# Kernel tuning notes

Measured on AMD Instinct MI355X. Metric: run time of the kernel, lower is better.

## Reference

```python
import math
import jax, jax.numpy as jnp
import numpy as np

WINDOW = 2  # LocalAttention default window_size
EPS = 1e-6


def _linear(x, W, b):
    return x @ W + b


def local_attention(x, Wq, bq, Wk, bk, Wv, bv):
    # x: [B, S, D]
    B, S, D = x.shape
    q = _linear(x, Wq, bq)
    k = _linear(x, Wk, bk)
    v = _linear(x, Wv, bv)
    idx = jnp.arange(S)
    # 0/1 banded mask -> softmax gives a dense row-stochastic matrix (faithful to source)
    mask = (jnp.abs(idx[:, None] - idx[None, :]) <= WINDOW).astype(x.dtype)  # [S, S]
    A = jax.nn.softmax(mask, axis=-1)  # [S, S]
    kk = jnp.einsum('st,btd->bsd', A, k)  # bmm(A, k)
    scores = jnp.einsum('bsd,btd->bst', q, kk) / math.sqrt(D)
    return jnp.einsum('bst,btd->bsd', jax.nn.softmax(scores, axis=-1), v)


def whole_norm(x, w, b):
    # LayerNorm with normalized_shape == full [B, S, D]: normalize over ALL elements
    mu = jnp.mean(x)
    var = jnp.mean(jnp.square(x - mu))
    return (x - mu) * jax.lax.rsqrt(var + EPS) * w + b


def ffn(x, W1, b1, W2, b2):
    return _linear(jax.nn.relu(_linear(x, W1, b1)), W2, b2)


def branch(feat, Wq, bq, Wk, bk, Wv, bv, W1, b1, W2, b2, nw, nb):
    out = local_attention(feat, Wq, bq, Wk, bk, Wv, bv)
    out = whole_norm(out + feat, nw, nb)
    out = ffn(out, W1, b1, W2, b2)
    return whole_norm(out + feat, nw, nb)


def _make_params(key, B, S, D):
    ks = jax.random.split(key, 5)
    s = 1.0 / math.sqrt(D)
    Wq = jax.random.normal(ks[0], (D, D), jnp.float32) * s
    Wk = jax.random.normal(ks[1], (D, D), jnp.float32) * s
    Wv = jax.random.normal(ks[2], (D, D), jnp.float32) * s
    W1 = jax.random.normal(ks[3], (D, 4 * D), jnp.float32) * s
    W2 = jax.random.normal(ks[4], (4 * D, D), jnp.float32) * (1.0 / math.sqrt(4 * D))
    return dict(Wq=Wq, bq=jnp.zeros((D,)), Wk=Wk, bk=jnp.zeros((D,)),
                Wv=Wv, bv=jnp.zeros((D,)), W1=W1, b1=jnp.zeros((4 * D,)),
                W2=W2, b2=jnp.zeros((D,)), nw=jnp.ones((B, S, D)), nb=jnp.zeros((B, S, D)))


def setup_inputs() -> dict:
    key = jax.random.key(0)
    k0, k1, k2, k3 = jax.random.split(key, 4)
    B, St, Dt = 8, 512, 1024
    Si, Di = 196, 768
    inp = {
        'text_feature': jax.random.normal(k0, (B, St, Dt), jnp.float32),
        'image_feature': jax.random.normal(k1, (B, Si, Di), jnp.float32),
    }
    tp = _make_params(k2, B, St, Dt)
    ip = _make_params(k3, B, Si, Di)
    for k, v in tp.items():
        inp['t_' + k] = v
    for k, v in ip.items():
        inp['i_' + k] = v
    return inp


def reference(text_feature, image_feature,
              t_Wq, t_bq, t_Wk, t_bk, t_Wv, t_bv, t_W1, t_b1, t_W2, t_b2, t_nw, t_nb,
              i_Wq, i_bq, i_Wk, i_bk, i_Wv, i_bv, i_W1, i_b1, i_W2, i_b2, i_nw, i_nb):
    image_out = branch(image_feature, i_Wq, i_bq, i_Wk, i_bk, i_Wv, i_bv,
                       i_W1, i_b1, i_W2, i_b2, i_nw, i_nb)
    text_out = branch(text_feature, t_Wq, t_bq, t_Wk, t_bk, t_Wv, t_bv,
                      t_W1, t_b1, t_W2, t_b2, t_nw, t_nb)
    return (text_out, image_out)
```

## Files before the change

kernel.cpp:

```cpp
#include <hip/hip_runtime.h>
#include <math.h>

typedef float  f32x4  __attribute__((ext_vector_type(4)));
typedef short  bf16x8 __attribute__((ext_vector_type(8)));

__device__ __forceinline__ unsigned short f2bf(float f) {
    union { float f; unsigned u; } v; v.f = f;
    unsigned u = v.u;
    return (unsigned short)((u + 0x7FFFu + ((u >> 16) & 1u)) >> 16);
}
__device__ __forceinline__ float bf2f(unsigned short u) {
    union { unsigned u; float f; } v; v.u = (unsigned)u << 16; return v.f;
}

#define GLOAD_LDS16(g, l)                                                      \
    __builtin_amdgcn_global_load_lds(                                          \
        (const __attribute__((address_space(1))) void*)(g),                    \
        (__attribute__((address_space(3))) void*)(l), 16, 0, 0)

template<int MR, int NR, bool OUT_BF16, bool RELU>
__global__ __launch_bounds__(512, 2)
void gemm2_bf16(const unsigned short* __restrict__ A,
                const unsigned short* __restrict__ BT,
                const float* __restrict__ bias, void* __restrict__ Cv,
                int M, int N, int K, int lda, int ldb, int ldc,
                long long sA, long long sB, long long sC, float alpha,
                int gx, int gy)
{
    constexpr int BK = 32;
    constexpr int WM = MR * 16, WN = NR * 16;
    constexpr int BM = 2 * WM, BN = 4 * WN;
    __shared__ unsigned short Asm[2][BM * BK];
    __shared__ unsigned short Bsm[2][BN * BK];

    A  += (long long)blockIdx.z * sA;
    BT += (long long)blockIdx.z * sB;
    char* Cb = (char*)Cv + (long long)blockIdx.z * sC * (OUT_BF16 ? 2 : 4);

    const int nwg = gx * gy;
    int orig = blockIdx.x;
    int xcd = orig & 7, sidx = orig >> 3;
    int qq = nwg >> 3, rr = nwg & 7;
    int wg = (xcd < rr ? xcd * (qq + 1) : rr * (qq + 1) + (xcd - rr) * qq) + sidx;
    const int row0 = (wg % gy) * BM;
    const int col0 = (wg / gy) * BN;

    const int tid  = threadIdx.x;
    const int lane = tid & 63;
    const int wave = tid >> 6;
    const int wr   = wave >> 2;
    const int wc   = wave & 3;

    const int srow = tid >> 2;
    const int skel = (tid & 3) * 8;

    const int lrow = lane & 15;
    const int lk   = (lane >> 4) * 8;

    f32x4 acc[MR][NR] = {};

    auto stage = [&](int buf, int k0) {
        #pragma unroll
        for (int is = 0; is < BM / 128; ++is)
            GLOAD_LDS16(A + (long long)(row0 + is * 128 + srow) * lda + (k0 + skel),
                        &Asm[buf][(is * 128 + srow) * BK + skel]);
        #pragma unroll
        for (int is = 0; is < BN / 128; ++is)
            GLOAD_LDS16(BT + (long long)(col0 + is * 128 + srow) * ldb + (k0 + skel),
                        &Bsm[buf][(is * 128 + srow) * BK + skel]);
    };

    const int nt = K / BK;
    stage(0, 0);
    __syncthreads();
    int cur = 0;
    for (int t = 0; t < nt; ++t) {
        if (t + 1 < nt) stage(cur ^ 1, (t + 1) * BK);

        bf16x8 af[MR], bfr[NR];
        #pragma unroll
        for (int mf = 0; mf < MR; ++mf)
            af[mf] = *(const bf16x8*)&Asm[cur][(wr * WM + mf * 16 + lrow) * BK + lk];
        #pragma unroll
        for (int nf = 0; nf < NR; ++nf)
            bfr[nf] = *(const bf16x8*)&Bsm[cur][(wc * WN + nf * 16 + lrow) * BK + lk];
        #pragma unroll
        for (int mf = 0; mf < MR; ++mf)
            #pragma unroll
            for (int nf = 0; nf < NR; ++nf)
                acc[mf][nf] = __builtin_amdgcn_mfma_f32_16x16x32_bf16(
                    af[mf], bfr[nf], acc[mf][nf], 0, 0, 0);

        __syncthreads();
        cur ^= 1;
    }

    const int crow = (lane >> 4) * 4;
    const int ccol = lane & 15;
    #pragma unroll
    for (int mf = 0; mf < MR; ++mf) {
        int rbase = row0 + wr * WM + mf * 16 + crow;
        #pragma unroll
        for (int nf = 0; nf < NR; ++nf) {
            int c = col0 + wc * WN + nf * 16 + ccol;
            if (c >= N) continue;
            float bv = bias ? bias[c] : 0.f;
            #pragma unroll
            for (int j = 0; j < 4; ++j) {
                int r = rbase + j;
                if (r >= M) continue;
                float v = acc[mf][nf][j] * alpha + bv;
                if (RELU) v = fmaxf(v, 0.f);
                if (OUT_BF16)
                    ((unsigned short*)Cb)[(long long)r * ldc + c] = f2bf(v);
                else
                    ((float*)Cb)[(long long)r * ldc + c] = v;
            }
        }
    }
}

template<int MR, int NR>
static void gemm2_t(bool outBf16, bool relu,
                    const unsigned short* A, const unsigned short* BT, const float* bias,
                    void* C, int M, int N, int K, int lda, int ldb, int ldc,
                    int batch, long long sA, long long sB, long long sC,
                    float alpha, hipStream_t st)
{
    const int BM = 2 * MR * 16, BN = 4 * NR * 16;
    int gx = (N + BN - 1) / BN, gy = (M + BM - 1) / BM;
    dim3 grid(gx * gy, 1, batch);
    if (outBf16) {
        if (relu) gemm2_bf16<MR, NR, true , true ><<<grid, 512, 0, st>>>(A, BT, bias, C, M, N, K, lda, ldb, ldc, sA, sB, sC, alpha, gx, gy);
        else      gemm2_bf16<MR, NR, true , false><<<grid, 512, 0, st>>>(A, BT, bias, C, M, N, K, lda, ldb, ldc, sA, sB, sC, alpha, gx, gy);
    } else {
        if (relu) gemm2_bf16<MR, NR, false, true ><<<grid, 512, 0, st>>>(A, BT, bias, C, M, N, K, lda, ldb, ldc, sA, sB, sC, alpha, gx, gy);
        else      gemm2_bf16<MR, NR, false, false><<<grid, 512, 0, st>>>(A, BT, bias, C, M, N, K, lda, ldb, ldc, sA, sB, sC, alpha, gx, gy);
    }
}

template<int BM, int BN, bool OUT_BF16>
__global__ __launch_bounds__(256)
void gemm_bf16(const unsigned short* __restrict__ A,
               const unsigned short* __restrict__ BT,
               const float* __restrict__ bias, void* __restrict__ Cv,
               int M, int N, int K, int lda, int ldb, int ldc,
               long long sA, long long sB, long long sC, float alpha,
               int gx, int gy)
{
    constexpr int BK = 32;
    constexpr int WM = BM / 2, WN = BN / 2;
    constexpr int MR = WM / 16, NR = WN / 16;
    __shared__ unsigned short Asm[BM * BK];
    __shared__ unsigned short Bsm[BN * BK];

    A  += (long long)blockIdx.z * sA;
    BT += (long long)blockIdx.z * sB;
    char* Cb = (char*)Cv + (long long)blockIdx.z * sC * (OUT_BF16 ? 2 : 4);

    const int nwg = gx * gy;
    int orig = blockIdx.x;
    int xcd = orig & 7, sidx = orig >> 3;
    int qq = nwg >> 3, rr = nwg & 7;
    int wg = (xcd < rr ? xcd * (qq + 1) : rr * (qq + 1) + (xcd - rr) * qq) + sidx;
    const int row0 = (wg % gy) * BM;
    const int col0 = (wg / gy) * BN;

    const int tid  = threadIdx.x;
    const int lane = tid & 63;
    const int wave = tid >> 6;
    const int wr   = wave >> 1;
    const int wc   = wave & 1;

    const int srow = tid >> 2;
    const int skel = (tid & 3) * 8;

    f32x4 acc[MR][NR] = {};

    const int lrow = lane & 15;
    const int lk   = (lane >> 4) * 8;

    for (int k0 = 0; k0 < K; k0 += BK) {
        #pragma unroll
        for (int is = 0; is < BM / 64; ++is)
            GLOAD_LDS16(A + (long long)(row0 + is * 64 + srow) * lda + (k0 + skel),
                        &Asm[(is * 64 + srow) * BK + skel]);
        #pragma unroll
        for (int is = 0; is < BN / 64; ++is)
            GLOAD_LDS16(BT + (long long)(col0 + is * 64 + srow) * ldb + (k0 + skel),
                        &Bsm[(is * 64 + srow) * BK + skel]);
        __syncthreads();

        bf16x8 af[MR], bfr[NR];
        #pragma unroll
        for (int mf = 0; mf < MR; ++mf)
            af[mf] = *(const bf16x8*)&Asm[(wr * WM + mf * 16 + lrow) * BK + lk];
        #pragma unroll
        for (int nf = 0; nf < NR; ++nf)
            bfr[nf] = *(const bf16x8*)&Bsm[(wc * WN + nf * 16 + lrow) * BK + lk];
        #pragma unroll
        for (int mf = 0; mf < MR; ++mf)
            #pragma unroll
            for (int nf = 0; nf < NR; ++nf)
                acc[mf][nf] = __builtin_amdgcn_mfma_f32_16x16x32_bf16(
                    af[mf], bfr[nf], acc[mf][nf], 0, 0, 0);
        __syncthreads();
    }

    const int crow = (lane >> 4) * 4;
    const int ccol = lane & 15;
    #pragma unroll
    for (int mf = 0; mf < MR; ++mf) {
        int rbase = row0 + wr * WM + mf * 16 + crow;
        #pragma unroll
        for (int nf = 0; nf < NR; ++nf) {
            int c = col0 + wc * WN + nf * 16 + ccol;
            if (c >= N) continue;
            float bv = bias ? bias[c] : 0.f;
            #pragma unroll
            for (int j = 0; j < 4; ++j) {
                int r = rbase + j;
                if (r >= M) continue;
                float v = acc[mf][nf][j] * alpha + bv;
                if (OUT_BF16)
                    ((unsigned short*)Cb)[(long long)r * ldc + c] = f2bf(v);
                else
                    ((float*)Cb)[(long long)r * ldc + c] = v;
            }
        }
    }
}

template<int BM, int BN>
static void gemm_t(bool outBf16,
                   const unsigned short* A, const unsigned short* BT, const float* bias,
                   void* C, int M, int N, int K, int lda, int ldb, int ldc,
                   int batch, long long sA, long long sB, long long sC,
                   float alpha, hipStream_t st)
{
    int gx = (N + BN - 1) / BN, gy = (M + BM - 1) / BM;
    dim3 grid(gx * gy, 1, batch);
    if (outBf16)
        gemm_bf16<BM, BN, true ><<<grid, 256, 0, st>>>(A, BT, bias, C, M, N, K, lda, ldb, ldc, sA, sB, sC, alpha, gx, gy);
    else
        gemm_bf16<BM, BN, false><<<grid, 256, 0, st>>>(A, BT, bias, C, M, N, K, lda, ldb, ldc, sA, sB, sC, alpha, gx, gy);
}

__global__ void splitk_stats_kernel(const float4* __restrict__ part,
                                    const float4* __restrict__ bias,
                                    const float4* __restrict__ x,
                                    float4* __restrict__ z,
                                    double* __restrict__ dpart,
                                    long long n4, int N4, int nsplit, long long stride4)
{
    __shared__ double rs[256], rs2[256];
    int tid = threadIdx.x;
    long long i = (long long)blockIdx.x * blockDim.x + tid;
    long long gs = (long long)gridDim.x * blockDim.x;
    double s = 0.0, s2 = 0.0;
    for (; i < n4; i += gs) {
        float4 a = part[i];
        for (int sp = 1; sp < nsplit; ++sp) {
            float4 b = part[(long long)sp * stride4 + i];
            a.x += b.x; a.y += b.y; a.z += b.z; a.w += b.w;
        }
        float4 bv = bias[(int)(i % N4)];
        float4 xv = x[i];
        a.x += bv.x + xv.x; a.y += bv.y + xv.y; a.z += bv.z + xv.z; a.w += bv.w + xv.w;
        z[i] = a;
        s  += (double)a.x + (double)a.y + (double)a.z + (double)a.w;
        s2 += (double)a.x * a.x + (double)a.y * a.y + (double)a.z * a.z + (double)a.w * a.w;
    }
    rs[tid] = s; rs2[tid] = s2; __syncthreads();
    for (int k = 128; k > 0; k >>= 1) {
        if (tid < k) { rs[tid] += rs[tid + k]; rs2[tid] += rs2[tid + k]; }
        __syncthreads();
    }
    if (tid == 0) { dpart[2 * blockIdx.x] = rs[0]; dpart[2 * blockIdx.x + 1] = rs2[0]; }
}

__global__ void norm_apply_z_kernel(const float4* __restrict__ z,
                                    const float4* __restrict__ nw, const float4* __restrict__ nb,
                                    const float* __restrict__ stats, float4* __restrict__ out,
                                    long long n4)
{
    float mu = stats[0], rstd = stats[1];
    long long i = (long long)blockIdx.x * blockDim.x + threadIdx.x;
    long long stride = (long long)gridDim.x * blockDim.x;
    for (; i < n4; i += stride) {
        float4 zv = z[i], wv = nw[i], bv = nb[i];
        float4 o;
        o.x = (zv.x - mu) * rstd * wv.x + bv.x;
        o.y = (zv.y - mu) * rstd * wv.y + bv.y;
        o.z = (zv.z - mu) * rstd * wv.z + bv.z;
        o.w = (zv.w - mu) * rstd * wv.w + bv.w;
        out[i] = o;
    }
}

__global__ void cast_bf16_kernel(const float4* __restrict__ in,
                                 ushort4* __restrict__ out, long long n4)
{
    long long i = (long long)blockIdx.x * blockDim.x + threadIdx.x;
    long long stride = (long long)gridDim.x * blockDim.x;
    for (; i < n4; i += stride) {
        float4 v = in[i];
        ushort4 o;
        o.x = f2bf(v.x); o.y = f2bf(v.y); o.z = f2bf(v.z); o.w = f2bf(v.w);
        out[i] = o;
    }
}

__global__ void transpose_cast_kernel(const float* __restrict__ src,
                                      unsigned short* __restrict__ dst,
                                      int R, int C, int Rpad,
                                      long long sSrc, long long sDst)
{
    __shared__ float t[32][33];
    src += (long long)blockIdx.z * sSrc;
    dst += (long long)blockIdx.z * sDst;
    int r0 = blockIdx.x * 32, c0 = blockIdx.y * 32;
    int tx = threadIdx.x & 31, ty = threadIdx.x >> 5;
    #pragma unroll
    for (int i = 0; i < 32; i += 8) {
        int r = r0 + ty + i, c = c0 + tx;
        t[ty + i][tx] = (r < R && c < C) ? src[(long long)r * C + c] : 0.f;
    }
    __syncthreads();
    #pragma unroll
    for (int i = 0; i < 32; i += 8) {
        int c = c0 + ty + i, r = r0 + tx;
        if (c < C && r < Rpad)
            dst[(long long)c * Rpad + r] = f2bf(t[tx][ty + i]);
    }
}

__global__ void transpose_bf16_kernel(const unsigned short* __restrict__ src,
                                      unsigned short* __restrict__ dst,
                                      int R, int C, int Rpad, int ldS,
                                      long long sSrc, long long sDst)
{
    __shared__ unsigned short t[32][33];
    src += (long long)blockIdx.z * sSrc;
    dst += (long long)blockIdx.z * sDst;
    int r0 = blockIdx.x * 32, c0 = blockIdx.y * 32;
    int tx = threadIdx.x & 31, ty = threadIdx.x >> 5;
    #pragma unroll
    for (int i = 0; i < 32; i += 8) {
        int r = r0 + ty + i, c = c0 + tx;
        t[ty + i][tx] = (r < R && c < C) ? src[(long long)r * ldS + c] : (unsigned short)0;
    }
    __syncthreads();
    #pragma unroll
    for (int i = 0; i < 32; i += 8) {
        int c = c0 + ty + i, r = r0 + tx;
        if (c < C && r < Rpad)
            dst[(long long)c * Rpad + r] = t[tx][ty + i];
    }
}

#define KTOT_NCH 16
__global__ void ktot_partial_bf16(const unsigned short* __restrict__ k,
                                  float* __restrict__ part,
                                  int B, int S, int D, int ld)
{
    int bch = blockIdx.x;
    int b  = bch / KTOT_NCH;
    int ch = bch % KTOT_NCH;
    int d  = blockIdx.y * 256 + threadIdx.x;
    if (d >= D) return;
    int len = (S + KTOT_NCH - 1) / KTOT_NCH;
    int lo = ch * len;
    int hi = lo + len < S ? lo + len : S;
    const unsigned short* kp = k + ((long long)b * S + lo) * ld + d;
    float s = 0.f;
    for (int t = lo; t < hi; ++t, kp += ld) s += bf2f(*kp);
    part[(long long)bch * D + d] = s;
}

__global__ void ktot_finish_kernel(const float* __restrict__ part,
                                   float* __restrict__ ktot, int B, int D)
{
    int idx = blockIdx.x * blockDim.x + threadIdx.x;
    if (idx >= B * D) return;
    int b = idx / D, d = idx % D;
    float s = 0.f;
    #pragma unroll
    for (int ch = 0; ch < KTOT_NCH; ++ch)
        s += part[((long long)b * KTOT_NCH + ch) * D + d];
    ktot[idx] = s;
}

__global__ void kk_bf16_kernel(const unsigned short* __restrict__ k,
                               const float* __restrict__ ktot,
                               unsigned short* __restrict__ kk,
                               int B, int S, int D, int ld)
{
    long long idx = (long long)blockIdx.x * blockDim.x + threadIdx.x;
    int D4 = D >> 2;
    long long n4 = (long long)B * S * D4;
    if (idx >= n4) return;
    int d4 = (int)(idx % D4);
    long long bs = idx / D4;
    int s = (int)(bs % S);
    int b = (int)(bs / S);
    int lo = s - 2 > 0 ? s - 2 : 0;
    int hi = s + 2 < S - 1 ? s + 2 : S - 1;
    int c = hi - lo + 1;
    const float E = 2.718281828459045f;
    float Zinv = 1.f / ((float)(S - c) + E * (float)c);

    float w0 = 0.f, w1 = 0.f, w2 = 0.f, w3 = 0.f;
    const unsigned short* kp = k + ((long long)b * S + lo) * ld + d4 * 4;
    for (int t = lo; t <= hi; ++t, kp += ld) {
        ushort4 kv = *(const ushort4*)kp;
        w0 += bf2f(kv.x); w1 += bf2f(kv.y); w2 += bf2f(kv.z); w3 += bf2f(kv.w);
    }
    float4 tot = *((const float4*)(ktot + b * D) + d4);
    ushort4 o;
    o.x = f2bf((tot.x + (E - 1.f) * w0) * Zinv);
    o.y = f2bf((tot.y + (E - 1.f) * w1) * Zinv);
    o.z = f2bf((tot.z + (E - 1.f) * w2) * Zinv);
    o.w = f2bf((tot.w + (E - 1.f) * w3) * Zinv);
    ((ushort4*)(kk + ((long long)b * S + s) * D))[d4] = o;
}

__global__ void softmax_rows_bf16(const float* __restrict__ sc,
                                  unsigned short* __restrict__ P, int S, int Spad)
{
    long long row = blockIdx.x;
    const float* p = sc + row * (long long)Spad;
    unsigned short* o = P + row * (long long)Spad;
    int tid = threadIdx.x;
    __shared__ float red[256];

    float m = -INFINITY;
    for (int t = tid; t < S; t += 256) m = fmaxf(m, p[t]);
    red[tid] = m; __syncthreads();
    for (int s = 128; s > 0; s >>= 1) {
        if (tid < s) red[tid] = fmaxf(red[tid], red[tid + s]);
        __syncthreads();
    }
    m = red[0];
    __syncthreads();

    float sum = 0.f;
    for (int t = tid; t < S; t += 256) sum += __expf(p[t] - m);
    red[tid] = sum; __syncthreads();
    for (int s = 128; s > 0; s >>= 1) {
        if (tid < s) red[tid] += red[tid + s];
        __syncthreads();
    }
    float inv = 1.f / red[0];
    for (int t = tid; t < Spad; t += 256)
        o[t] = (t < S) ? f2bf(__expf(p[t] - m) * inv) : (unsigned short)0;
}

__global__ void stats_kernel(const float4* __restrict__ a, const float4* __restrict__ f,
                             double* __restrict__ part, long long n4)
{
    __shared__ double rs[256], rs2[256];
    int tid = threadIdx.x;
    long long i = (long long)blockIdx.x * blockDim.x + tid;
    long long stride = (long long)gridDim.x * blockDim.x;
    double s = 0.0, s2 = 0.0;
    for (; i < n4; i += stride) {
        float4 av = a[i], fv = f[i];
        float z0 = av.x + fv.x, z1 = av.y + fv.y, z2 = av.z + fv.z, z3 = av.w + fv.w;
        s  += (double)z0 + (double)z1 + (double)z2 + (double)z3;
        s2 += (double)z0 * z0 + (double)z1 * z1 + (double)z2 * z2 + (double)z3 * z3;
    }
    rs[tid] = s; rs2[tid] = s2; __syncthreads();
    for (int k = 128; k > 0; k >>= 1) {
        if (tid < k) { rs[tid] += rs[tid + k]; rs2[tid] += rs2[tid + k]; }
        __syncthreads();
    }
    if (tid == 0) { part[2 * blockIdx.x] = rs[0]; part[2 * blockIdx.x + 1] = rs2[0]; }
}

__global__ void finish_stats(const double* __restrict__ part, int npart,
                             float* __restrict__ stats, double n)
{
    __shared__ double rs[256], rs2[256];
    int tid = threadIdx.x;
    double s = 0.0, s2 = 0.0;
    for (int i = tid; i < npart; i += 256) { s += part[2 * i]; s2 += part[2 * i + 1]; }
    rs[tid] = s; rs2[tid] = s2; __syncthreads();
    for (int k = 128; k > 0; k >>= 1) {
        if (tid < k) { rs[tid] += rs[tid + k]; rs2[tid] += rs2[tid + k]; }
        __syncthreads();
    }
    if (tid == 0) {
        double mu  = rs[0] / n;
        double var = rs2[0] / n - mu * mu;
        stats[0] = (float)mu;
        stats[1] = (float)(1.0 / sqrt(var + 1e-6));
    }
}

__global__ void norm_apply_kernel(const float4* __restrict__ a, const float4* __restrict__ f,
                                  const float4* __restrict__ nw, const float4* __restrict__ nb,
                                  const float* __restrict__ stats, ushort4* __restrict__ out,
                                  long long n4)
{
    float mu = stats[0], rstd = stats[1];
    long long i = (long long)blockIdx.x * blockDim.x + threadIdx.x;
    long long stride = (long long)gridDim.x * blockDim.x;
    for (; i < n4; i += stride) {
        float4 av = a[i], fv = f[i], wv = nw[i], bv = nb[i];
        ushort4 o;
        o.x = f2bf((av.x + fv.x - mu) * rstd * wv.x + bv.x);
        o.y = f2bf((av.y + fv.y - mu) * rstd * wv.y + bv.y);
        o.z = f2bf((av.z + fv.z - mu) * rstd * wv.z + bv.z);
        o.w = f2bf((av.w + fv.w - mu) * rstd * wv.w + bv.w);
        out[i] = o;
    }
}

struct Bufs {
    unsigned short *xb, *qkv, *kkb, *vT, *P, *h, *WqkvT, *W1T, *W2T;
    float *f32buf, *bqkv, *ktot, *ktot_part, *stats;
    double *part;
};

static void run_branch(const float* x, const float* const* w, bool big,
                       float* out, int B, int S, int D, const Bufs& wsb, hipStream_t st)
{
    const float *Wq = w[0], *bq = w[1], *Wk = w[2], *bk = w[3], *Wv = w[4], *bv = w[5];
    const float *W1 = w[6], *b1 = w[7], *W2 = w[8], *b2 = w[9], *nw = w[10], *nb = w[11];

    const int Spad = (S + 31) & ~31;
    const long long M = (long long)B * S;
    const long long n = M * D;
    const long long n4 = n / 4;
    const float inv_sqrt_d = (float)(1.0 / sqrt((double)D));
    const int D3 = 3 * D, D4 = 4 * D;

    unsigned short* y1b = wsb.kkb;
    float* scores = (float*)wsb.h;
    float* splitbuf = (float*)wsb.qkv;

    cast_bf16_kernel<<<1024, 256, 0, st>>>((const float4*)x, (ushort4*)wsb.xb, n4);
    transpose_cast_kernel<<<dim3((D + 31) / 32, (D + 31) / 32, 1), 256, 0, st>>>(Wq, wsb.WqkvT,               D, D, D, 0, 0);
    transpose_cast_kernel<<<dim3((D + 31) / 32, (D + 31) / 32, 1), 256, 0, st>>>(Wk, wsb.WqkvT + (long long)D * D, D, D, D, 0, 0);
    transpose_cast_kernel<<<dim3((D + 31) / 32, (D + 31) / 32, 1), 256, 0, st>>>(Wv, wsb.WqkvT + 2LL * D * D, D, D, D, 0, 0);
    transpose_cast_kernel<<<dim3((D + 31) / 32, (D4 + 31) / 32, 1), 256, 0, st>>>(W1, wsb.W1T, D, D4, D, 0, 0);
    transpose_cast_kernel<<<dim3((D4 + 31) / 32, (D + 31) / 32, 1), 256, 0, st>>>(W2, wsb.W2T, D4, D, D4, 0, 0);
    hipMemcpyAsync(wsb.bqkv,         bq, D * sizeof(float), hipMemcpyDeviceToDevice, st);
    hipMemcpyAsync(wsb.bqkv + D,     bk, D * sizeof(float), hipMemcpyDeviceToDevice, st);
    hipMemcpyAsync(wsb.bqkv + 2 * D, bv, D * sizeof(float), hipMemcpyDeviceToDevice, st);

    if (big)
        gemm2_t<8, 2>(true, false, wsb.xb, wsb.WqkvT, wsb.bqkv, wsb.qkv,
                      (int)M, D3, D, D, D, D3, 1, 0, 0, 0, 1.f, st);
    else
        gemm2_t<4, 2>(true, false, wsb.xb, wsb.WqkvT, wsb.bqkv, wsb.qkv,
                      (int)M, D3, D, D, D, D3, 1, 0, 0, 0, 1.f, st);

    const unsigned short* kcol = wsb.qkv + D;
    ktot_partial_bf16<<<dim3(B * KTOT_NCH, (D + 255) / 256), 256, 0, st>>>(kcol, wsb.ktot_part, B, S, D, D3);
    ktot_finish_kernel<<<(B * D + 255) / 256, 256, 0, st>>>(wsb.ktot_part, wsb.ktot, B, D);
    kk_bf16_kernel<<<(int)((n4 + 255) / 256), 256, 0, st>>>(kcol, wsb.ktot, wsb.kkb, B, S, D, D3);

    transpose_bf16_kernel<<<dim3((Spad + 31) / 32, (D + 31) / 32, B), 256, 0, st>>>(
        wsb.qkv + 2 * D, wsb.vT, S, D, Spad, D3, (long long)S * D3, (long long)D * Spad);

    gemm_t<64, 64>(false, wsb.qkv, wsb.kkb, nullptr, scores, S, S, D, D3, D, Spad,
                   B, (long long)S * D3, (long long)S * D, (long long)S * Spad, inv_sqrt_d, st);
    softmax_rows_bf16<<<(int)M, 256, 0, st>>>(scores, wsb.P, S, Spad);

    gemm_t<128, 64>(false, wsb.P, wsb.vT, nullptr, wsb.f32buf, S, D, Spad, Spad, Spad, D,
                    B, (long long)S * Spad, (long long)D * Spad, (long long)S * D, 1.f, st);

    stats_kernel<<<1024, 256, 0, st>>>((const float4*)wsb.f32buf, (const float4*)x, wsb.part, n4);
    finish_stats<<<1, 256, 0, st>>>(wsb.part, 1024, wsb.stats, (double)n);
    norm_apply_kernel<<<2048, 256, 0, st>>>((const float4*)wsb.f32buf, (const float4*)x,
        (const float4*)nw, (const float4*)nb, wsb.stats, (ushort4*)y1b, n4);

    if (big)
        gemm2_t<8, 4>(true, true, y1b, wsb.W1T, b1, wsb.h, (int)M, D4, D, D, D, D4, 1, 0, 0, 0, 1.f, st);
    else
        gemm2_t<4, 2>(true, true, y1b, wsb.W1T, b1, wsb.h, (int)M, D4, D, D, D, D4, 1, 0, 0, 0, 1.f, st);

    {
        int nsplit = big ? 2 : 4;
        int Ksp = D4 / nsplit;
        if (big)
            gemm2_t<8, 2>(false, false, wsb.h, wsb.W2T, nullptr, splitbuf,
                          (int)M, D, Ksp, D4, D4, D,
                          nsplit, Ksp, Ksp, M * D, 1.f, st);
        else
            gemm2_t<4, 2>(false, false, wsb.h, wsb.W2T, nullptr, splitbuf,
                          (int)M, D, Ksp, D4, D4, D,
                          nsplit, Ksp, Ksp, M * D, 1.f, st);
        splitk_stats_kernel<<<1024, 256, 0, st>>>((const float4*)splitbuf, (const float4*)b2,
                                                  (const float4*)x, (float4*)wsb.f32buf,
                                                  wsb.part, n4, D / 4, nsplit, n4);
        finish_stats<<<1, 256, 0, st>>>(wsb.part, 1024, wsb.stats, (double)n);
        norm_apply_z_kernel<<<2048, 256, 0, st>>>((const float4*)wsb.f32buf,
            (const float4*)nw, (const float4*)nb, wsb.stats, (float4*)out, n4);
    }
}

extern "C" void kernel_launch(void* const* d_in, const int* in_sizes, int n_in,
                              void* d_out, int out_size, void* d_ws, size_t ws_size,
                              hipStream_t stream)
{
    const float* text  = (const float*)d_in[0];
    const float* image = (const float*)d_in[1];
    const float* tw[12];
    const float* iw[12];
    for (int i = 0; i < 12; ++i) tw[i] = (const float*)d_in[2 + i];
    for (int i = 0; i < 12; ++i) iw[i] = (const float*)d_in[14 + i];

    float* out_text = (float*)d_out;
    float* out_img  = out_text + 8LL * 512 * 1024;

    char* p = (char*)d_ws;
    auto alloc = [&](long long bytes) {
        char* r = p;
        p += (bytes + 255) & ~255LL;
        return r;
    };
    const long long MD  = 4096LL * 1024;
    const long long BDS = 8LL * 1024 * 512;
    const long long SS  = 8LL * 512 * 512;
    Bufs b;
    b.xb      = (unsigned short*)alloc(MD * 2);
    b.qkv     = (unsigned short*)alloc(MD * 3 * 2);
    b.kkb     = (unsigned short*)alloc(MD * 2);
    b.vT      = (unsigned short*)alloc(BDS * 2);
    b.P       = (unsigned short*)alloc(SS * 2);
    b.h       = (unsigned short*)alloc(MD * 4 * 2);
    b.WqkvT   = (unsigned short*)alloc(3LL * 1024 * 1024 * 2);
    b.W1T     = (unsigned short*)alloc(4096LL * 1024 * 2);
    b.W2T     = (unsigned short*)alloc(4096LL * 1024 * 2);
    b.f32buf  = (float*)alloc(MD * 4);
    b.bqkv    = (float*)alloc(3LL * 1024 * 4);
    b.ktot    = (float*)alloc(8192LL * 4);
    b.ktot_part = (float*)alloc(8192LL * KTOT_NCH * 4);
    b.part    = (double*)alloc(2048LL * 8);
    b.stats   = (float*)alloc(256);

    run_branch(text,  tw, true,  out_text, 8, 512, 1024, b, stream);
    run_branch(image, iw, false, out_img,  8, 196, 768,  b, stream);
}
```

Baseline: 503.3 us.

## Add BK=64 swizzled 256-row GEMM kernel for big-branch QKV and FFN matmuls

Introduces a new bf16 MFMA GEMM with 256-row tiles, a K-step of 64 and XOR-swizzled LDS layout, and uses it for the text branch's QKV, FFN1 and split-K FFN2 GEMMs. It also changes tile rasterization to row-major over gx, raises gemm2's launch-bounds occupancy hint to 4, and doubles split-K for the small image branch. The aim is more data reuse per tile, fewer LDS bank conflicts and better occupancy and parallelism. The cost is larger LDS use per block and more register pressure, and the epilogue stores are scalar and unvectorised.

```diff
diff --git a/kernel.cpp b/kernel.cpp
--- a/kernel.cpp
+++ b/kernel.cpp
@@ -18,8 +18,139 @@
         (const __attribute__((address_space(1))) void*)(g),                    \
         (__attribute__((address_space(3))) void*)(l), 16, 0, 0)
 
+template<int NR, bool OUT_BF16, bool RELU>
+__global__ __launch_bounds__(512, 2)
+void gemm3_bf16(const unsigned short* __restrict__ A,
+                const unsigned short* __restrict__ BT,
+                const float* __restrict__ bias, void* __restrict__ Cv,
+                int M, int N, int K, int lda, int ldb, int ldc,
+                long long sA, long long sB, long long sC, float alpha,
+                int gx, int gy)
+{
+    constexpr int MR = 8;
+    constexpr int BK = 64;
+    constexpr int BM = 256, BN = NR * 64;
+    constexpr int WN = NR * 16;
+    __shared__ unsigned short Asm[2][BM * BK];
+    __shared__ unsigned short Bsm[2][BN * BK];
+
+    A  += (long long)blockIdx.z * sA;
+    BT += (long long)blockIdx.z * sB;
+    char* Cb = (char*)Cv + (long long)blockIdx.z * sC * (OUT_BF16 ? 2 : 4);
+
+    const int nwg = gx * gy;
+    int orig = blockIdx.x;
+    int xcd = orig & 7, sidx = orig >> 3;
+    int qq = nwg >> 3, rr = nwg & 7;
+    int wg = (xcd < rr ? xcd * (qq + 1) : rr * (qq + 1) + (xcd - rr) * qq) + sidx;
+    const int row0 = (wg / gx) * BM;
+    const int col0 = (wg % gx) * BN;
+
+    const int tid  = threadIdx.x;
+    const int lane = tid & 63;
+    const int wave = tid >> 6;
+    const int wr   = wave >> 2;
+    const int wc   = wave & 3;
+
+    const int lrow = lane & 15;
+    const int cgrp = lane >> 4;
+
+    f32x4 acc[MR][NR] = {};
+
+    const int srl = tid >> 3;
+    const int scl = (tid & 7) ^ (srl & 7);
+
+    auto stage = [&](int buf, int k0) {
+        #pragma unroll
+        for (int is = 0; is < BM / 64; ++is)
+            GLOAD_LDS16(A + (long long)(row0 + is * 64 + srl) * lda + (k0 + scl * 8),
+                        &Asm[buf][is * 64 * BK + tid * 8]);
+        #pragma unroll
+        for (int is = 0; is < BN / 64; ++is)
+            GLOAD_LDS16(BT + (long long)(col0 + is * 64 + srl) * ldb + (k0 + scl * 8),
+                        &Bsm[buf][is * 64 * BK + tid * 8]);
+    };
+
+    const int nt = K / BK;
+    stage(0, 0);
+    __syncthreads();
+
+    for (int t = 0; t < nt; ++t) {
+        if (t + 1 < nt) stage((t + 1) & 1, (t + 1) * BK);
+        const int cur = t & 1;
+
+        #pragma unroll
+        for (int kk = 0; kk < 2; ++kk) {
+            bf16x8 a_[MR];
+            #pragma unroll
+            for (int mf = 0; mf < MR; ++mf) {
+                int row = wr * 128 + mf * 16 + lrow;
+                int phys = (kk * 4 + cgrp) ^ (row & 7);
+                a_[mf] = *(const bf16x8*)&Asm[cur][row * BK + phys * 8];
+            }
+            bf16x8 b_[NR];
+            #pragma unroll
+            for (int nf = 0; nf < NR; ++nf) {
+                int row = wc * WN + nf * 16 + lrow;
+                int phys = (kk * 4 + cgrp) ^ (row & 7);
+                b_[nf] = *(const bf16x8*)&Bsm[cur][row * BK + phys * 8];
+            }
+            #pragma unroll
+            for (int mf = 0; mf < MR; ++mf)
+                #pragma unroll
+                for (int nf = 0; nf < NR; ++nf)
+                    acc[mf][nf] = __builtin_amdgcn_mfma_f32_16x16x32_bf16(
+                        a_[mf], b_[nf], acc[mf][nf], 0, 0, 0);
+        }
+        __syncthreads();
+    }
+
+    const int crow = cgrp * 4;
+    const int ccol = lane & 15;
+    #pragma unroll
+    for (int mf = 0; mf < MR; ++mf) {
+        int rbase = row0 + wr * 128 + mf * 16 + crow;
+        #pragma unroll
+        for (int nf = 0; nf < NR; ++nf) {
+            int c = col0 + wc * WN + nf * 16 + ccol;
+            if (c >= N) continue;
+            float bv = bias ? bias[c] : 0.f;
+            #pragma unroll
+            for (int j = 0; j < 4; ++j) {
+                int r = rbase + j;
+                if (r >= M) continue;
+                float v = acc[mf][nf][j] * alpha + bv;
+                if (RELU) v = fmaxf(v, 0.f);
+                if (OUT_BF16)
+                    ((unsigned short*)Cb)[(long long)r * ldc + c] = f2bf(v);
+                else
+                    ((float*)Cb)[(long long)r * ldc + c] = v;
+            }
+        }
+    }
+}
+
+template<int NR>
+static void gemm3_t(bool outBf16, bool relu,
+                    const unsigned short* A, const unsigned short* BT, const float* bias,
+                    void* C, int M, int N, int K, int lda, int ldb, int ldc,
+                    int batch, long long sA, long long sB, long long sC,
+                    float alpha, hipStream_t st)
+{
+    const int BM = 256, BN = NR * 64;
+    int gx = (N + BN - 1) / BN, gy = (M + BM - 1) / BM;
+    dim3 grid(gx * gy, 1, batch);
+    if (outBf16) {
+        if (relu) gemm3_bf16<NR, true , true ><<<grid, 512, 0, st>>>(A, BT, bias, C, M, N, K, lda, ldb, ldc, sA, sB, sC, alpha, gx, gy);
+        else      gemm3_bf16<NR, true , false><<<grid, 512, 0, st>>>(A, BT, bias, C, M, N, K, lda, ldb, ldc, sA, sB, sC, alpha, gx, gy);
+    } else {
+        if (relu) gemm3_bf16<NR, false, true ><<<grid, 512, 0, st>>>(A, BT, bias, C, M, N, K, lda, ldb, ldc, sA, sB, sC, alpha, gx, gy);
+        else      gemm3_bf16<NR, false, false><<<grid, 512, 0, st>>>(A, BT, bias, C, M, N, K, lda, ldb, ldc, sA, sB, sC, alpha, gx, gy);
+    }
+}
+
 template<int MR, int NR, bool OUT_BF16, bool RELU>
-__global__ __launch_bounds__(512, 2)
+__global__ __launch_bounds__(512, 4)
 void gemm2_bf16(const unsigned short* __restrict__ A,
                 const unsigned short* __restrict__ BT,
                 const float* __restrict__ bias, void* __restrict__ Cv,
@@ -42,8 +173,8 @@
     int xcd = orig & 7, sidx = orig >> 3;
     int qq = nwg >> 3, rr = nwg & 7;
     int wg = (xcd < rr ? xcd * (qq + 1) : rr * (qq + 1) + (xcd - rr) * qq) + sidx;
-    const int row0 = (wg % gy) * BM;
-    const int col0 = (wg / gy) * BN;
+    const int row0 = (wg / gx) * BM;
+    const int col0 = (wg % gx) * BN;
 
     const int tid  = threadIdx.x;
     const int lane = tid & 63;
@@ -551,8 +682,8 @@
     hipMemcpyAsync(wsb.bqkv + 2 * D, bv, D * sizeof(float), hipMemcpyDeviceToDevice, st);
 
     if (big)
-        gemm2_t<8, 2>(true, false, wsb.xb, wsb.WqkvT, wsb.bqkv, wsb.qkv,
-                      (int)M, D3, D, D, D, D3, 1, 0, 0, 0, 1.f, st);
+        gemm3_t<4>(true, false, wsb.xb, wsb.WqkvT, wsb.bqkv, wsb.qkv,
+                   (int)M, D3, D, D, D, D3, 1, 0, 0, 0, 1.f, st);
     else
         gemm2_t<4, 2>(true, false, wsb.xb, wsb.WqkvT, wsb.bqkv, wsb.qkv,
                       (int)M, D3, D, D, D, D3, 1, 0, 0, 0, 1.f, st);
@@ -578,17 +709,17 @@
         (const float4*)nw, (const float4*)nb, wsb.stats, (ushort4*)y1b, n4);
 
     if (big)
-        gemm2_t<8, 4>(true, true, y1b, wsb.W1T, b1, wsb.h, (int)M, D4, D, D, D, D4, 1, 0, 0, 0, 1.f, st);
+        gemm3_t<4>(true, true, y1b, wsb.W1T, b1, wsb.h, (int)M, D4, D, D, D, D4, 1, 0, 0, 0, 1.f, st);
     else
         gemm2_t<4, 2>(true, true, y1b, wsb.W1T, b1, wsb.h, (int)M, D4, D, D, D, D4, 1, 0, 0, 0, 1.f, st);
 
     {
-        int nsplit = big ? 2 : 4;
+        int nsplit = big ? 2 : 8;
         int Ksp = D4 / nsplit;
         if (big)
-            gemm2_t<8, 2>(false, false, wsb.h, wsb.W2T, nullptr, splitbuf,
-                          (int)M, D, Ksp, D4, D4, D,
-                          nsplit, Ksp, Ksp, M * D, 1.f, st);
+            gemm3_t<2>(false, false, wsb.h, wsb.W2T, nullptr, splitbuf,
+                       (int)M, D, Ksp, D4, D4, D,
+                       nsplit, Ksp, Ksp, M * D, 1.f, st);
         else
             gemm2_t<4, 2>(false, false, wsb.h, wsb.W2T, nullptr, splitbuf,
                           (int)M, D, Ksp, D4, D4, D,
```

Measured after the change: 483.1 us. -4.0%, faster.
